# Performance work log

Hardware: AMD Instinct MI355X
Metric: run time of the kernel (lower is better)

## Reference

```python
import jax, jax.numpy as jnp
import numpy as np

B, N, C, H = 2, 2048, 256, 8
HD = C // H  # 32


def _pairwise_sq_dist(x, y):
    # x,y: [B,N,3] -> [B,N,N] squared euclidean distance
    x2 = jnp.sum(x * x, axis=-1)  # [B,N]
    y2 = jnp.sum(y * y, axis=-1)  # [B,N]
    xy = jnp.einsum('bnd,bmd->bnm', x, y)
    return x2[:, :, None] + y2[:, None, :] - 2.0 * xy


def setup_inputs() -> dict:
    key = jax.random.key(0)
    ks = jax.random.split(key, 12)
    s = 0.02
    return {
        'feature': jax.random.normal(ks[0], (B, N, C), jnp.float32),
        'points': jax.random.normal(ks[1], (B, N, 3), jnp.float32),
        'Wq': jax.random.normal(ks[2], (C, H * HD), jnp.float32) * s,
        'bq': jnp.zeros((H * HD,), jnp.float32),
        'Wk': jax.random.normal(ks[3], (C, H * HD), jnp.float32) * s,
        'bk': jnp.zeros((H * HD,), jnp.float32),
        'Wv': jax.random.normal(ks[4], (C, H * HD), jnp.float32) * s,
        'bv': jnp.zeros((H * HD,), jnp.float32),
        'Wo': jax.random.normal(ks[5], (H * HD, C), jnp.float32) * s,
        'bo': jnp.zeros((C,), jnp.float32),
        'ln_g': jnp.ones((C,), jnp.float32),
        'ln_b': jnp.zeros((C,), jnp.float32),
    }


def reference(feature, points, Wq, bq, Wk, bk, Wv, bv, Wo, bo, ln_g, ln_b):
    xyz = points[..., 0:3]
    dist = _pairwise_sq_dist(xyz, xyz)  # [B,N,N] geometric bias

    q = (feature @ Wq + bq).reshape(B, N, H, HD)
    k = (feature @ Wk + bk).reshape(B, N, H, HD)
    v = (feature @ Wv + bv).reshape(B, N, H, HD)

    # distance-biased multi-head attention (Geoglobal_FPT)
    logits = jnp.einsum('bnhd,bmhd->bhnm', q, k) / jnp.sqrt(jnp.float32(HD))
    logits = logits - dist[:, None, :, :]  # closer points attend more
    attn = jax.nn.softmax(logits, axis=-1)
    out = jnp.einsum('bhnm,bmhd->bnhd', attn, v).reshape(B, N, H * HD)
    out = out @ Wo + bo

    # residual + post-LayerNorm
    f = feature + out
    mu = jnp.mean(f, axis=-1, keepdims=True)
    var = jnp.mean(jnp.square(f - mu), axis=-1, keepdims=True)
    f = (f - mu) * jax.lax.rsqrt(var + 1e-5) * ln_g + ln_b
    return f
```

## Files before the change

kernel.cpp:

```cpp
#include <hip/hip_runtime.h>
#include <hip/hip_bf16.h>

#define B_ 2
#define N_ 2048
#define C_ 256
#define H_ 8
#define HD_ 32

typedef __bf16 bhalf;
typedef bhalf bhalf8 __attribute__((ext_vector_type(8)));
typedef bhalf bhalf4 __attribute__((ext_vector_type(4)));
typedef float floatx4 __attribute__((ext_vector_type(4)));

__global__ __launch_bounds__(256) void prep_w(
    const float* __restrict__ Wq, const float* __restrict__ Wk,
    const float* __restrict__ Wv, const float* __restrict__ Wo,
    bhalf* __restrict__ Wtb)
{
    __shared__ float T[64][65];
    const float* W = blockIdx.y == 0 ? Wq : (blockIdx.y == 1 ? Wk : (blockIdx.y == 2 ? Wv : Wo));
    bhalf* dst = Wtb + (size_t)blockIdx.y * (C_ * C_);
    const int kt = (blockIdx.x >> 2) * 64, nt = (blockIdx.x & 3) * 64;
    const int t = threadIdx.x;
    const int c4 = (t & 15) * 4;
#pragma unroll
    for (int i = 0; i < 4; ++i) {
        const int r = (t >> 4) + i * 16;
        const float4 w = *(const float4*)&W[(kt + r) * C_ + nt + c4];
        T[r][c4 + 0] = w.x; T[r][c4 + 1] = w.y; T[r][c4 + 2] = w.z; T[r][c4 + 3] = w.w;
    }
    __syncthreads();
#pragma unroll
    for (int i = 0; i < 4; ++i) {
        const int n = (t >> 4) + i * 16;
        bhalf4 o;
        o[0] = (bhalf)T[c4 + 0][n]; o[1] = (bhalf)T[c4 + 1][n];
        o[2] = (bhalf)T[c4 + 2][n]; o[3] = (bhalf)T[c4 + 3][n];
        *(bhalf4*)&dst[(nt + n) * C_ + kt + c4] = o;
    }
}

__global__ __launch_bounds__(256) void prep_ext(
    const float* __restrict__ pts, bhalf* __restrict__ qext, bhalf* __restrict__ kext)
{
    const int i = blockIdx.x * 256 + threadIdx.x;
    const float x = pts[i * 3 + 0], y = pts[i * 3 + 1], z = pts[i * 3 + 2];
    const float nn = x * x + y * y + z * z;
    const bhalf hi = (bhalf)nn;
    const bhalf lo = (bhalf)(nn - (float)hi);
    bhalf8 qe, ke;
    qe[0] = (bhalf)(2.f * x); qe[1] = (bhalf)(2.f * y); qe[2] = (bhalf)(2.f * z);
    qe[3] = (bhalf)(-(float)hi); qe[4] = (bhalf)(-(float)lo);
    qe[5] = (bhalf)1.f; qe[6] = (bhalf)1.f; qe[7] = (bhalf)0.f;
    ke[0] = (bhalf)x; ke[1] = (bhalf)y; ke[2] = (bhalf)z;
    ke[3] = (bhalf)1.f; ke[4] = (bhalf)1.f;
    ke[5] = (bhalf)(-(float)hi); ke[6] = (bhalf)(-(float)lo); ke[7] = (bhalf)0.f;
    *(bhalf8*)&qext[(size_t)i * 8] = qe;
    *(bhalf8*)&kext[(size_t)i * 8] = ke;
}

__global__ __launch_bounds__(256) void qkv_gemm(
    const float* __restrict__ feat, const bhalf* __restrict__ Wtb,
    const float* __restrict__ bq, const float* __restrict__ bk,
    const float* __restrict__ bv,
    bhalf* __restrict__ qs, bhalf* __restrict__ kg, bhalf* __restrict__ vt)
{
    __shared__ __align__(16) bhalf Alds[64][72];
    __shared__ __align__(16) bhalf Blds[64][72];

    const int tid = threadIdx.x;
    const int wave = tid >> 6, lane = tid & 63;
    const int quad = lane >> 4, l16 = lane & 15;
    const int m0 = blockIdx.x * 64;
    const int which = blockIdx.y >> 2;
    const int n0 = (blockIdx.y & 3) * 64;
    const bhalf* Wt = Wtb + (size_t)which * (C_ * C_);
    const float* bias = which == 0 ? bq : (which == 1 ? bk : bv);

    const floatx4 zacc = {0.f, 0.f, 0.f, 0.f};
    floatx4 acc[4];
#pragma unroll
    for (int f = 0; f < 4; ++f) acc[f] = zacc;

    const int ar = tid >> 2, aseg = tid & 3;

    for (int kc = 0; kc < C_; kc += 64) {
        __syncthreads();
        {
            const float* fp = &feat[(m0 + ar) * C_ + kc + aseg * 16];
            const float4 a0 = *(const float4*)(fp);
            const float4 a1 = *(const float4*)(fp + 4);
            const float4 a2 = *(const float4*)(fp + 8);
            const float4 a3 = *(const float4*)(fp + 12);
            bhalf8 v0, v1;
            v0[0] = (bhalf)a0.x; v0[1] = (bhalf)a0.y; v0[2] = (bhalf)a0.z; v0[3] = (bhalf)a0.w;
            v0[4] = (bhalf)a1.x; v0[5] = (bhalf)a1.y; v0[6] = (bhalf)a1.z; v0[7] = (bhalf)a1.w;
            v1[0] = (bhalf)a2.x; v1[1] = (bhalf)a2.y; v1[2] = (bhalf)a2.z; v1[3] = (bhalf)a2.w;
            v1[4] = (bhalf)a3.x; v1[5] = (bhalf)a3.y; v1[6] = (bhalf)a3.z; v1[7] = (bhalf)a3.w;
            *(bhalf8*)&Alds[ar][aseg * 16] = v0;
            *(bhalf8*)&Alds[ar][aseg * 16 + 8] = v1;
            const bhalf* wp = &Wt[(n0 + ar) * C_ + kc + aseg * 16];
            *(bhalf8*)&Blds[ar][aseg * 16] = *(const bhalf8*)(wp);
            *(bhalf8*)&Blds[ar][aseg * 16 + 8] = *(const bhalf8*)(wp + 8);
        }
        __syncthreads();
        const bhalf8 af0 = *(const bhalf8*)&Alds[wave * 16 + l16][quad * 8];
        const bhalf8 af1 = *(const bhalf8*)&Alds[wave * 16 + l16][32 + quad * 8];
#pragma unroll
        for (int f = 0; f < 4; ++f) {
            const bhalf8 b0 = *(const bhalf8*)&Blds[f * 16 + l16][quad * 8];
            const bhalf8 b1 = *(const bhalf8*)&Blds[f * 16 + l16][32 + quad * 8];
            acc[f] = __builtin_amdgcn_mfma_f32_16x16x32_bf16(af0, b0, acc[f], 0, 0, 0);
            acc[f] = __builtin_amdgcn_mfma_f32_16x16x32_bf16(af1, b1, acc[f], 0, 0, 0);
        }
    }

    const float scale = 0.17677669529663687f;
#pragma unroll
    for (int f = 0; f < 4; ++f) {
        const int cg = n0 + f * 16 + l16;
        const float bi = bias[cg];
        const int hh = cg >> 5, dd = cg & 31;
#pragma unroll
        for (int r = 0; r < 4; ++r) {
            const int m = m0 + wave * 16 + quad * 4 + r;
            const int bb = m >> 11, nn = m & (N_ - 1);
            const float val = acc[f][r] + bi;
            if (which == 0) {
                qs[((size_t)(bb * H_ + hh) * N_ + nn) * HD_ + dd] = (bhalf)(val * scale);
            } else if (which == 1) {
                kg[((size_t)(bb * H_ + hh) * N_ + nn) * HD_ + dd] = (bhalf)val;
            } else {
                vt[(((size_t)(bb * H_ + hh) * (N_ / 64) + (nn >> 6)) * HD_ + dd) * 64 + (nn & 63)] = (bhalf)val;
            }
        }
    }
}

__global__ __launch_bounds__(256) void attn_kernel(
    const bhalf* __restrict__ qs, const bhalf* __restrict__ kg,
    const bhalf* __restrict__ vt, const bhalf* __restrict__ qext,
    const bhalf* __restrict__ kext,
    bhalf* __restrict__ po, float* __restrict__ pl, int spbits)
{
    __shared__ __align__(16) bhalf Ks[64][40];
    __shared__ __align__(16) bhalf Vts[32][72];
    __shared__ __align__(16) bhalf Plds[4][16][72];

    const int tid = threadIdx.x;
    const int wave = tid >> 6, lane = tid & 63;
    const int quad = lane >> 4, l16 = lane & 15;
    const int n0 = blockIdx.x * 64;
    const int h = blockIdx.y;
    const int sp = blockIdx.z & ((1 << spbits) - 1);
    const int b = blockIdx.z >> spbits;
    const int bh = b * H_ + h;

    const int qrow = n0 + wave * 16 + l16;
    const bhalf8 aq = *(const bhalf8*)&qs[((size_t)bh * N_ + qrow) * HD_ + quad * 8];
    bhalf8 aq2;
    {
        const bhalf8 qe = *(const bhalf8*)&qext[(size_t)(b * N_ + qrow) * 8];
        bhalf8 zv;
#pragma unroll
        for (int j = 0; j < 8; ++j) zv[j] = (bhalf)0.f;
        aq2 = (quad == 0) ? qe : zv;
    }

    const floatx4 zacc = {0.f, 0.f, 0.f, 0.f};
    floatx4 o0 = zacc, o1 = zacc;
    float ls[4] = {0.f, 0.f, 0.f, 0.f};

    const int skey = tid >> 2, sseg = tid & 3;
    const int vd = tid >> 3, vks = tid & 7;
    const int iters = (N_ >> spbits) / 64;
    const int mbase = sp * (N_ >> spbits);

    for (int it = 0; it < iters; ++it) {
        const int m0 = mbase + it * 64;
        __syncthreads();
        *(bhalf8*)&Ks[skey][sseg * 8] =
            *(const bhalf8*)&kg[((size_t)bh * N_ + m0 + skey) * HD_ + sseg * 8];
        *(bhalf8*)&Vts[vd][vks * 8] =
            *(const bhalf8*)&vt[(((size_t)bh * (N_ / 64) + (m0 >> 6)) * HD_ + vd) * 64 + vks * 8];
        __syncthreads();

#pragma unroll
        for (int s4 = 0; s4 < 4; ++s4) {
            const bhalf8 bk_ = *(const bhalf8*)&Ks[s4 * 16 + l16][quad * 8];
            floatx4 s = __builtin_amdgcn_mfma_f32_16x16x32_bf16(aq, bk_, zacc, 0, 0, 0);
            const bhalf8 ke = *(const bhalf8*)&kext[(size_t)(b * N_ + m0 + s4 * 16 + l16) * 8];
            s = __builtin_amdgcn_mfma_f32_16x16x32_bf16(aq2, ke, s, 0, 0, 0);
#pragma unroll
            for (int r = 0; r < 4; ++r) {
                const float p = __expf(s[r]);
                ls[r] += p;
                Plds[wave][quad * 4 + r][s4 * 16 + l16] = (bhalf)p;
            }
        }
        const bhalf8 ap0 = *(const bhalf8*)&Plds[wave][l16][quad * 8];
        const bhalf8 ap1 = *(const bhalf8*)&Plds[wave][l16][32 + quad * 8];
        const bhalf8 bv00 = *(const bhalf8*)&Vts[l16][quad * 8];
        const bhalf8 bv01 = *(const bhalf8*)&Vts[l16][32 + quad * 8];
        const bhalf8 bv10 = *(const bhalf8*)&Vts[16 + l16][quad * 8];
        const bhalf8 bv11 = *(const bhalf8*)&Vts[16 + l16][32 + quad * 8];
        o0 = __builtin_amdgcn_mfma_f32_16x16x32_bf16(ap0, bv00, o0, 0, 0, 0);
        o0 = __builtin_amdgcn_mfma_f32_16x16x32_bf16(ap1, bv01, o0, 0, 0, 0);
        o1 = __builtin_amdgcn_mfma_f32_16x16x32_bf16(ap0, bv10, o1, 0, 0, 0);
        o1 = __builtin_amdgcn_mfma_f32_16x16x32_bf16(ap1, bv11, o1, 0, 0, 0);
    }

    const size_t pobase = (size_t)sp * ((size_t)B_ * H_ * N_ * HD_) + (size_t)bh * N_ * HD_;
#pragma unroll
    for (int r = 0; r < 4; ++r) {
        float s = ls[r];
        s += __shfl_xor(s, 1); s += __shfl_xor(s, 2);
        s += __shfl_xor(s, 4); s += __shfl_xor(s, 8);
        const int row = n0 + wave * 16 + quad * 4 + r;
        po[pobase + (size_t)row * HD_ + l16] = (bhalf)o0[r];
        po[pobase + (size_t)row * HD_ + l16 + 16] = (bhalf)o1[r];
        if (l16 == 0)
            pl[(size_t)sp * (B_ * H_ * N_) + (size_t)bh * N_ + row] = s;
    }
}

__global__ __launch_bounds__(256) void outln_gemm(
    const bhalf* __restrict__ po, const float* __restrict__ pl,
    const bhalf* __restrict__ Wot, const float* __restrict__ bo,
    const float* __restrict__ feat, const float* __restrict__ g,
    const float* __restrict__ bb, float* __restrict__ out, int splits)
{
    __shared__ __align__(16) bhalf Alds[16][264];
    __shared__ __align__(16) bhalf Blds[256][40];
    __shared__ float rden[16][8];
    __shared__ float wsum[4][16][2];
    __shared__ float stats[16][2];

    const int tid = threadIdx.x;
    const int wave = tid >> 6, lane = tid & 63;
    const int quad = lane >> 4, l16 = lane & 15;
    const int row0 = blockIdx.x * 16;

    if (tid < 128) {
        const int m = tid >> 3, hh = tid & 7;
        const int grow = row0 + m;
        const int b = grow >> 11, n = grow & (N_ - 1);
        float den = 0.f;
        for (int sp = 0; sp < splits; ++sp)
            den += pl[(size_t)sp * (B_ * H_ * N_) + (size_t)(b * H_ + hh) * N_ + n];
        rden[m][hh] = 1.f / den;
    }
    __syncthreads();

    {
        const int m = tid >> 4, seg = tid & 15;
        const int hh = seg >> 1, d0 = (seg & 1) * 16;
        const int grow = row0 + m;
        const int b = grow >> 11, n = grow & (N_ - 1);
        const size_t idx = ((size_t)(b * H_ + hh) * N_ + n) * HD_ + d0;
        float num[16];
#pragma unroll
        for (int j = 0; j < 16; ++j) num[j] = 0.f;
        for (int sp = 0; sp < splits; ++sp) {
            const bhalf8 p0 = *(const bhalf8*)&po[(size_t)sp * ((size_t)B_ * H_ * N_ * HD_) + idx];
            const bhalf8 p1 = *(const bhalf8*)&po[(size_t)sp * ((size_t)B_ * H_ * N_ * HD_) + idx + 8];
#pragma unroll
            for (int j = 0; j < 8; ++j) { num[j] += (float)p0[j]; num[8 + j] += (float)p1[j]; }
        }
        const float r = rden[m][hh];
        bhalf8 a0, a1;
#pragma unroll
        for (int j = 0; j < 8; ++j) { a0[j] = (bhalf)(num[j] * r); a1[j] = (bhalf)(num[8 + j] * r); }
        *(bhalf8*)&Alds[m][seg * 16] = a0;
        *(bhalf8*)&Alds[m][seg * 16 + 8] = a1;
    }

    const floatx4 zacc = {0.f, 0.f, 0.f, 0.f};
    floatx4 acc[4];
#pragma unroll
    for (int f = 0; f < 4; ++f) acc[f] = zacc;

    for (int kc = 0; kc < C_; kc += 32) {
        __syncthreads();
        {
            const bhalf* wp = &Wot[tid * C_ + kc];
            *(bhalf8*)&Blds[tid][0]  = *(const bhalf8*)(wp);
            *(bhalf8*)&Blds[tid][8]  = *(const bhalf8*)(wp + 8);
            *(bhalf8*)&Blds[tid][16] = *(const bhalf8*)(wp + 16);
            *(bhalf8*)&Blds[tid][24] = *(const bhalf8*)(wp + 24);
        }
        __syncthreads();
        const bhalf8 af = *(const bhalf8*)&Alds[l16][kc + quad * 8];
#pragma unroll
        for (int f = 0; f < 4; ++f) {
            const bhalf8 bfr = *(const bhalf8*)&Blds[wave * 64 + f * 16 + l16][quad * 8];
            acc[f] = __builtin_amdgcn_mfma_f32_16x16x32_bf16(af, bfr, acc[f], 0, 0, 0);
        }
    }

    float fv[4][4];
    float s1[4] = {0.f, 0.f, 0.f, 0.f}, s2[4] = {0.f, 0.f, 0.f, 0.f};
#pragma unroll
    for (int f = 0; f < 4; ++f) {
        const int col = wave * 64 + f * 16 + l16;
        const float bic = bo[col];
#pragma unroll
        for (int r = 0; r < 4; ++r) {
            const int m = quad * 4 + r;
            const float x = acc[f][r] + bic + feat[(row0 + m) * C_ + col];
            fv[f][r] = x;
            s1[r] += x; s2[r] += x * x;
        }
    }
#pragma unroll
    for (int r = 0; r < 4; ++r) {
        for (int o = 1; o < 16; o <<= 1) {
            s1[r] += __shfl_xor(s1[r], o);
            s2[r] += __shfl_xor(s2[r], o);
        }
    }
    if (l16 == 0) {
#pragma unroll
        for (int r = 0; r < 4; ++r) {
            wsum[wave][quad * 4 + r][0] = s1[r];
            wsum[wave][quad * 4 + r][1] = s2[r];
        }
    }
    __syncthreads();
    if (tid < 16) {
        float a = 0.f, bsq = 0.f;
#pragma unroll
        for (int w = 0; w < 4; ++w) { a += wsum[w][tid][0]; bsq += wsum[w][tid][1]; }
        const float mu = a * (1.f / C_);
        const float var = bsq * (1.f / C_) - mu * mu;
        stats[tid][0] = mu;
        stats[tid][1] = rsqrtf(var + 1e-5f);
    }
    __syncthreads();
#pragma unroll
    for (int f = 0; f < 4; ++f) {
        const int col = wave * 64 + f * 16 + l16;
        const float gc = g[col], bc = bb[col];
#pragma unroll
        for (int r = 0; r < 4; ++r) {
            const int m = quad * 4 + r;
            out[(row0 + m) * C_ + col] = (fv[f][r] - stats[m][0]) * stats[m][1] * gc + bc;
        }
    }
}

extern "C" void kernel_launch(void* const* d_in, const int* in_sizes, int n_in,
                              void* d_out, int out_size, void* d_ws, size_t ws_size,
                              hipStream_t stream) {
    const float* feat = (const float*)d_in[0];
    const float* pts  = (const float*)d_in[1];
    const float* Wq   = (const float*)d_in[2];
    const float* bq   = (const float*)d_in[3];
    const float* Wk   = (const float*)d_in[4];
    const float* bk   = (const float*)d_in[5];
    const float* Wv   = (const float*)d_in[6];
    const float* bv   = (const float*)d_in[7];
    const float* Wo   = (const float*)d_in[8];
    const float* bo   = (const float*)d_in[9];
    const float* lng  = (const float*)d_in[10];
    const float* lnb  = (const float*)d_in[11];

    char* w = (char*)d_ws;
    bhalf* Wtb  = (bhalf*)(w);
    bhalf* qs   = (bhalf*)(w + 524288);
    bhalf* kg   = (bhalf*)(w + 2621440);
    bhalf* vtp  = (bhalf*)(w + 4718592);
    bhalf* qext = (bhalf*)(w + 6815744);
    bhalf* kext = (bhalf*)(w + 6881280);
    float* pl   = (float*)(w + 6946816);
    bhalf* po   = (bhalf*)(w + 7471104);

    const int spbits = (ws_size >= 15859712u) ? 2 : 1;
    const int splits = 1 << spbits;

    prep_w<<<dim3(16, 4), 256, 0, stream>>>(Wq, Wk, Wv, Wo, Wtb);
    prep_ext<<<B_ * N_ / 256, 256, 0, stream>>>(pts, qext, kext);
    qkv_gemm<<<dim3(B_ * N_ / 64, 12), 256, 0, stream>>>(
        feat, Wtb, bq, bk, bv, qs, kg, vtp);
    attn_kernel<<<dim3(N_ / 64, H_, B_ << spbits), 256, 0, stream>>>(
        qs, kg, vtp, qext, kext, po, pl, spbits);
    outln_gemm<<<B_ * N_ / 16, 256, 0, stream>>>(
        po, pl, Wtb + 3 * (C_ * C_), bo, feat, lng, lnb, (float*)d_out, splits);
}
```

Before: 143.5 us.

## Compute transposed scores so P stays in registers for PV MFMA

The attention kernel now computes S^T (keys as rows, queries as columns), so each lane's exp'd probabilities line up with the B-operand layout of a 16x16x16 bf16 MFMA. P no longer goes through the per-wave LDS buffer before the PV product, which removes LDS stores, loads and the related layout shuffle. The output is V^T·P^T accumulated per query column, giving vectorized bhalf4 output stores and a simpler row-sum reduction. In exchange it uses twice as many smaller-K MFMAs for PV and adds a compile-time fallback for the builtin name.

```diff
diff --git a/kernel.cpp b/kernel.cpp
--- a/kernel.cpp
+++ b/kernel.cpp
@@ -11,6 +11,16 @@
 typedef bhalf bhalf8 __attribute__((ext_vector_type(8)));
 typedef bhalf bhalf4 __attribute__((ext_vector_type(4)));
 typedef float floatx4 __attribute__((ext_vector_type(4)));
+typedef short short4v __attribute__((ext_vector_type(4)));
+
+__device__ __forceinline__ floatx4 mfma16x16x16bf16(bhalf4 a, bhalf4 b, floatx4 c) {
+#if __has_builtin(__builtin_amdgcn_mfma_f32_16x16x16_bf16)
+    return __builtin_amdgcn_mfma_f32_16x16x16_bf16(a, b, c, 0, 0, 0);
+#else
+    return __builtin_amdgcn_mfma_f32_16x16x16bf16_1k(
+        __builtin_bit_cast(short4v, a), __builtin_bit_cast(short4v, b), c, 0, 0, 0);
+#endif
+}
 
 __global__ __launch_bounds__(256) void prep_w(
     const float* __restrict__ Wq, const float* __restrict__ Wk,
@@ -145,7 +155,6 @@
 {
     __shared__ __align__(16) bhalf Ks[64][40];
     __shared__ __align__(16) bhalf Vts[32][72];
-    __shared__ __align__(16) bhalf Plds[4][16][72];
 
     const int tid = threadIdx.x;
     const int wave = tid >> 6, lane = tid & 63;
@@ -157,19 +166,16 @@
     const int bh = b * H_ + h;
 
     const int qrow = n0 + wave * 16 + l16;
-    const bhalf8 aq = *(const bhalf8*)&qs[((size_t)bh * N_ + qrow) * HD_ + quad * 8];
-    bhalf8 aq2;
-    {
-        const bhalf8 qe = *(const bhalf8*)&qext[(size_t)(b * N_ + qrow) * 8];
-        bhalf8 zv;
-#pragma unroll
-        for (int j = 0; j < 8; ++j) zv[j] = (bhalf)0.f;
-        aq2 = (quad == 0) ? qe : zv;
-    }
+    const bhalf8 bq_ = *(const bhalf8*)&qs[((size_t)bh * N_ + qrow) * HD_ + quad * 8];
+    bhalf8 zv8;
+#pragma unroll
+    for (int j = 0; j < 8; ++j) zv8[j] = (bhalf)0.f;
+    const bhalf8 bqe = (quad == 0)
+        ? *(const bhalf8*)&qext[(size_t)(b * N_ + qrow) * 8] : zv8;
 
     const floatx4 zacc = {0.f, 0.f, 0.f, 0.f};
     floatx4 o0 = zacc, o1 = zacc;
-    float ls[4] = {0.f, 0.f, 0.f, 0.f};
+    float ls = 0.f;
 
     const int skey = tid >> 2, sseg = tid & 3;
     const int vd = tid >> 3, vks = tid & 7;
@@ -186,42 +192,37 @@
         __syncthreads();
 
 #pragma unroll
-        for (int s4 = 0; s4 < 4; ++s4) {
-            const bhalf8 bk_ = *(const bhalf8*)&Ks[s4 * 16 + l16][quad * 8];
-            floatx4 s = __builtin_amdgcn_mfma_f32_16x16x32_bf16(aq, bk_, zacc, 0, 0, 0);
-            const bhalf8 ke = *(const bhalf8*)&kext[(size_t)(b * N_ + m0 + s4 * 16 + l16) * 8];
-            s = __builtin_amdgcn_mfma_f32_16x16x32_bf16(aq2, ke, s, 0, 0, 0);
+        for (int mt = 0; mt < 4; ++mt) {
+            const bhalf8 ak_ = *(const bhalf8*)&Ks[mt * 16 + l16][quad * 8];
+            floatx4 st = __builtin_amdgcn_mfma_f32_16x16x32_bf16(ak_, bq_, zacc, 0, 0, 0);
+            const bhalf8 ake = (quad == 0)
+                ? *(const bhalf8*)&kext[(size_t)(b * N_ + m0 + mt * 16 + l16) * 8] : zv8;
+            st = __builtin_amdgcn_mfma_f32_16x16x32_bf16(ake, bqe, st, 0, 0, 0);
+            bhalf4 pt;
 #pragma unroll
             for (int r = 0; r < 4; ++r) {
-                const float p = __expf(s[r]);
-                ls[r] += p;
-                Plds[wave][quad * 4 + r][s4 * 16 + l16] = (bhalf)p;
+                const float p = __expf(st[r]);
+                ls += p;
+                pt[r] = (bhalf)p;
             }
-        }
-        const bhalf8 ap0 = *(const bhalf8*)&Plds[wave][l16][quad * 8];
-        const bhalf8 ap1 = *(const bhalf8*)&Plds[wave][l16][32 + quad * 8];
-        const bhalf8 bv00 = *(const bhalf8*)&Vts[l16][quad * 8];
-        const bhalf8 bv01 = *(const bhalf8*)&Vts[l16][32 + quad * 8];
-        const bhalf8 bv10 = *(const bhalf8*)&Vts[16 + l16][quad * 8];
-        const bhalf8 bv11 = *(const bhalf8*)&Vts[16 + l16][32 + quad * 8];
-        o0 = __builtin_amdgcn_mfma_f32_16x16x32_bf16(ap0, bv00, o0, 0, 0, 0);
-        o0 = __builtin_amdgcn_mfma_f32_16x16x32_bf16(ap1, bv01, o0, 0, 0, 0);
-        o1 = __builtin_amdgcn_mfma_f32_16x16x32_bf16(ap0, bv10, o1, 0, 0, 0);
-        o1 = __builtin_amdgcn_mfma_f32_16x16x32_bf16(ap1, bv11, o1, 0, 0, 0);
-    }
+            const bhalf4 av0 = *(const bhalf4*)&Vts[l16][mt * 16 + quad * 4];
+            const bhalf4 av1 = *(const bhalf4*)&Vts[16 + l16][mt * 16 + quad * 4];
+            o0 = mfma16x16x16bf16(av0, pt, o0);
+            o1 = mfma16x16x16bf16(av1, pt, o1);
+        }
+    }
+
+    ls += __shfl_xor(ls, 16);
+    ls += __shfl_xor(ls, 32);
 
     const size_t pobase = (size_t)sp * ((size_t)B_ * H_ * N_ * HD_) + (size_t)bh * N_ * HD_;
-#pragma unroll
-    for (int r = 0; r < 4; ++r) {
-        float s = ls[r];
-        s += __shfl_xor(s, 1); s += __shfl_xor(s, 2);
-        s += __shfl_xor(s, 4); s += __shfl_xor(s, 8);
-        const int row = n0 + wave * 16 + quad * 4 + r;
-        po[pobase + (size_t)row * HD_ + l16] = (bhalf)o0[r];
-        po[pobase + (size_t)row * HD_ + l16 + 16] = (bhalf)o1[r];
-        if (l16 == 0)
-            pl[(size_t)sp * (B_ * H_ * N_) + (size_t)bh * N_ + row] = s;
-    }
+    bhalf4 w0, w1;
+#pragma unroll
+    for (int r = 0; r < 4; ++r) { w0[r] = (bhalf)o0[r]; w1[r] = (bhalf)o1[r]; }
+    *(bhalf4*)&po[pobase + (size_t)qrow * HD_ + quad * 4] = w0;
+    *(bhalf4*)&po[pobase + (size_t)qrow * HD_ + 16 + quad * 4] = w1;
+    if (lane < 16)
+        pl[(size_t)sp * (B_ * H_ * N_) + (size_t)bh * N_ + qrow] = ls;
 }
 
 __global__ __launch_bounds__(256) void outln_gemm(
```

New measurement: 132.3 us. 1.08x faster.
